# Performance work log

Measured on AMD Instinct MI355X. Metric: run time of the kernel, lower is better.

Reference implementation:

```python
import jax, jax.numpy as jnp
import numpy as np

# Synthetic layered DAG: 8 node-layers of width N -> 7 masked dense layers.
B = 4096        # batch
N = 2048        # nodes per DAG layer (= in_features = out_features)
DEPTH = 7       # number of weight layers (len(L) - 1)
DENSITY = 0.25  # fraction of predecessor edges present (mask sparsity)


def setup_inputs() -> dict:
    key = jax.random.key(0)
    kx, kw, km = jax.random.split(key, 3)
    x = jax.random.normal(kx, (B, N), dtype=jnp.float32)
    # Mask M: [DEPTH, N+1, N]; random 0/1 edges, last row (bias) all ones.
    m = (jax.random.uniform(km, (DEPTH, N + 1, N)) < DENSITY).astype(jnp.float32)
    M = m.at[:, -1, :].set(1.0)
    # Kaiming-uniform per column: bound = 1/sqrt(nnz_j) (torch code's init),
    # nonzero only at masked positions (W initialized to zeros elsewhere).
    nnz = jnp.maximum(M.sum(axis=1, keepdims=True), 1.0)  # [DEPTH,1,N]
    u = jax.random.uniform(kw, (DEPTH, N + 1, N), minval=-1.0, maxval=1.0)
    W = (u / jnp.sqrt(nnz)) * M
    return {"x": x, "W": W, "M": M}


def reference(x, W, M):
    # activations buffer semantics collapse to a per-layer chain because each
    # layer's preds are exactly the previous DAG layer; sinks = last layer.
    def step(acts, wm):
        w, m = wm  # [N+1, N] each
        h = jnp.concatenate(
            [acts, jnp.ones((acts.shape[0], 1), acts.dtype)], axis=1)  # [B, N+1]
        acts = jax.nn.relu(h @ (m * w))  # masked dense matmul + ReLU
        return acts, None

    out, _ = jax.lax.scan(step, x, (W, M))
    return out  # [B, N] activations of sink nodes
```

## Files before the change

### kernel.cpp

```cpp
#include <hip/hip_runtime.h>
#include <hip/hip_bf16.h>

typedef __bf16 bf16_t;
typedef __bf16 v8bf __attribute__((ext_vector_type(8)));
typedef __bf16 v4bf __attribute__((ext_vector_type(4)));
typedef float  v4f  __attribute__((ext_vector_type(4)));

#define B_ROWS 4096
#define N_COLS 2048
#define K_FULL 2049
#define K_PAD  2176
#define DEPTH  7

#define BM 128
#define BN 128
#define BK 64
#define NT (K_PAD / BK)

__global__ __launch_bounds__(256) void wt_kernel(const float* __restrict__ W,
                                                 bf16_t* __restrict__ Wt) {
  __shared__ float t[64][65];
  const int l  = blockIdx.z;
  const int k0 = blockIdx.x * 64;
  const int n0 = blockIdx.y * 64;
  const int tid = threadIdx.x;
  const int r  = tid >> 4;
  const int c4 = (tid & 15) * 4;
  const float* Wl = W + (size_t)l * K_FULL * N_COLS;
#pragma unroll
  for (int it = 0; it < 4; ++it) {
    const int k = k0 + r + it * 16;
    float4 v = make_float4(0.f, 0.f, 0.f, 0.f);
    if (k < K_FULL) v = *(const float4*)&Wl[(size_t)k * N_COLS + n0 + c4];
    t[c4 + 0][r + it * 16] = v.x;
    t[c4 + 1][r + it * 16] = v.y;
    t[c4 + 2][r + it * 16] = v.z;
    t[c4 + 3][r + it * 16] = v.w;
  }
  __syncthreads();
  bf16_t* Wtl = Wt + (size_t)l * N_COLS * K_PAD;
#pragma unroll
  for (int it = 0; it < 4; ++it) {
    const int n = r + it * 16;
    v4bf o;
    o[0] = (bf16_t)t[n][c4 + 0];
    o[1] = (bf16_t)t[n][c4 + 1];
    o[2] = (bf16_t)t[n][c4 + 2];
    o[3] = (bf16_t)t[n][c4 + 3];
    *(v4bf*)&Wtl[(size_t)(n0 + n) * K_PAD + k0 + c4] = o;
  }
}

__global__ __launch_bounds__(256) void init_kernel(const float* __restrict__ x,
                                                   bf16_t* __restrict__ A0,
                                                   bf16_t* __restrict__ A1) {
  const int c4 = (blockIdx.x * 256 + threadIdx.x) * 4;
  const int r  = blockIdx.y;
  if (c4 >= K_PAD) return;
  v4bf o;
  if (c4 < N_COLS) {
    const float4 v = *(const float4*)&x[(size_t)r * N_COLS + c4];
    o[0] = (bf16_t)v.x; o[1] = (bf16_t)v.y; o[2] = (bf16_t)v.z; o[3] = (bf16_t)v.w;
  } else {
    o[0] = (bf16_t)(c4 == N_COLS ? 1.0f : 0.0f);
    o[1] = (bf16_t)0.0f; o[2] = (bf16_t)0.0f; o[3] = (bf16_t)0.0f;
  }
  *(v4bf*)&A0[(size_t)r * K_PAD + c4] = o;
  if (c4 >= N_COLS) *(v4bf*)&A1[(size_t)r * K_PAD + c4] = o;
}

__global__ __launch_bounds__(256, 2) void gemm_kernel(
    const bf16_t* __restrict__ A, const bf16_t* __restrict__ Bt,
    bf16_t* __restrict__ Cn, float* __restrict__ Co) {
  __shared__ __align__(16) bf16_t As[2][BM * BK];
  __shared__ __align__(16) bf16_t Bs[2][BN * BK];

  const int tid  = threadIdx.x;
  const int wave = tid >> 6;
  const int lane = tid & 63;
  const int m0 = blockIdx.y * BM;
  const int n0 = blockIdx.x * BN;
  const int wm = (wave & 1) * 64;
  const int wn = (wave >> 1) * 64;
  const int quad = lane >> 4;
  const int l16  = lane & 15;

  int aoff[4], boff[4];
#pragma unroll
  for (int c = 0; c < 4; ++c) {
    const int gran = wave * 256 + c * 64 + lane;
    const int srow = gran >> 3;
    const int scol = ((gran & 7) ^ (srow & 7)) << 3;
    aoff[c] = (m0 + srow) * K_PAD + scol;
    boff[c] = (n0 + srow) * K_PAD + scol;
  }

  auto stage = [&](int buf, int kb) {
#pragma unroll
    for (int c = 0; c < 4; ++c) {
      __builtin_amdgcn_global_load_lds(
          (const __attribute__((address_space(1))) void*)(A + aoff[c] + kb),
          (__attribute__((address_space(3))) void*)((char*)&As[buf][0] + wave * 4096 + c * 1024),
          16, 0, 0);
    }
#pragma unroll
    for (int c = 0; c < 4; ++c) {
      __builtin_amdgcn_global_load_lds(
          (const __attribute__((address_space(1))) void*)(Bt + boff[c] + kb),
          (__attribute__((address_space(3))) void*)((char*)&Bs[buf][0] + wave * 4096 + c * 1024),
          16, 0, 0);
    }
  };

  v4f acc[4][4] = {};

  stage(0, 0);
  __syncthreads();

#pragma unroll 2
  for (int kt = 0; kt < NT; ++kt) {
    const int cur = kt & 1;
    if (kt + 1 < NT) stage(cur ^ 1, (kt + 1) * BK);

#pragma unroll
    for (int ks = 0; ks < 2; ++ks) {
      v8bf af[4], bfr[4];
      const int kg = ks * 4 + quad;
#pragma unroll
      for (int i = 0; i < 4; ++i) {
        const int arow = wm + i * 16 + l16;
        af[i] = *(const v8bf*)&As[cur][arow * BK + ((kg ^ (arow & 7)) << 3)];
      }
#pragma unroll
      for (int j = 0; j < 4; ++j) {
        const int brow = wn + j * 16 + l16;
        bfr[j] = *(const v8bf*)&Bs[cur][brow * BK + ((kg ^ (brow & 7)) << 3)];
      }
#pragma unroll
      for (int i = 0; i < 4; ++i)
#pragma unroll
        for (int j = 0; j < 4; ++j)
          acc[i][j] = __builtin_amdgcn_mfma_f32_16x16x32_bf16(af[i], bfr[j],
                                                              acc[i][j], 0, 0, 0);
    }
    __syncthreads();
  }

#pragma unroll
  for (int i = 0; i < 4; ++i) {
#pragma unroll
    for (int j = 0; j < 4; ++j) {
#pragma unroll
      for (int r = 0; r < 4; ++r) {
        float v = acc[i][j][r];
        v = v > 0.0f ? v : 0.0f;
        const int row = m0 + wm + i * 16 + quad * 4 + r;
        const int col = n0 + wn + j * 16 + l16;
        if (Co) Co[(size_t)row * N_COLS + col] = v;
        else    Cn[(size_t)row * K_PAD + col] = (bf16_t)v;
      }
    }
  }
}

extern "C" void kernel_launch(void* const* d_in, const int* in_sizes, int n_in,
                              void* d_out, int out_size, void* d_ws, size_t ws_size,
                              hipStream_t stream) {
  const float* x = (const float*)d_in[0];
  const float* W = (const float*)d_in[1];
  float* out = (float*)d_out;

  char* ws = (char*)d_ws;
  const size_t wtBytes = (size_t)DEPTH * N_COLS * K_PAD * sizeof(bf16_t);
  const size_t aBytes  = (size_t)B_ROWS * K_PAD * sizeof(bf16_t);
  bf16_t* Wt = (bf16_t*)ws;
  bf16_t* A0 = (bf16_t*)(ws + wtBytes);
  bf16_t* A1 = (bf16_t*)(ws + wtBytes + aBytes);

  wt_kernel<<<dim3(K_PAD / 64, N_COLS / 64, DEPTH), 256, 0, stream>>>(W, Wt);
  init_kernel<<<dim3((K_PAD / 4 + 255) / 256, B_ROWS), 256, 0, stream>>>(x, A0, A1);

  bf16_t* bufs[2] = {A0, A1};
  for (int l = 0; l < DEPTH; ++l) {
    const bf16_t* Ain = bufs[l & 1];
    bf16_t* Aout      = bufs[(l + 1) & 1];
    const bf16_t* Bl  = Wt + (size_t)l * N_COLS * K_PAD;
    const bool last   = (l == DEPTH - 1);
    gemm_kernel<<<dim3(N_COLS / BN, B_ROWS / BM), 256, 0, stream>>>(
        Ain, Bl, last ? nullptr : Aout, last ? out : nullptr);
  }
}
```

Measured before the change: 541.3 us.

## Use 128x256 tiles with 8 waves and half-K-tile software pipeline

The GEMM tile grows from 128x128 to 128x256, with 512 threads (8 waves) per block. Each K tile is staged in two 32-wide halves into a double buffer, so the next half-tile's global-to-LDS loads overlap the MFMAs, and explicit vmcnt waits and barriers replace the blanket syncthreads. A new quad-granular LDS swizzle and s_setprio around the MFMA block aim to cut bank conflicts and favour the math waves. The cost is 96KB of LDS per block, which may limit occupancy, plus fragile hand-written wait counts.

```diff
diff --git a/kernel.cpp b/kernel.cpp
--- a/kernel.cpp
+++ b/kernel.cpp
@@ -13,7 +13,7 @@
 #define DEPTH  7
 
 #define BM 128
-#define BN 128
+#define BN 256
 #define BK 64
 #define NT (K_PAD / BK)
 
@@ -69,82 +69,95 @@
   if (c4 >= N_COLS) *(v4bf*)&A1[(size_t)r * K_PAD + c4] = o;
 }
 
-__global__ __launch_bounds__(256, 2) void gemm_kernel(
+__global__ __launch_bounds__(512, 2) void gemm_kernel(
     const bf16_t* __restrict__ A, const bf16_t* __restrict__ Bt,
     bf16_t* __restrict__ Cn, float* __restrict__ Co) {
-  __shared__ __align__(16) bf16_t As[2][BM * BK];
-  __shared__ __align__(16) bf16_t Bs[2][BN * BK];
+  __shared__ __align__(16) char smem[2 * 49152];
 
   const int tid  = threadIdx.x;
   const int wave = tid >> 6;
   const int lane = tid & 63;
   const int m0 = blockIdx.y * BM;
   const int n0 = blockIdx.x * BN;
-  const int wm = (wave & 1) * 64;
-  const int wn = (wave >> 1) * 64;
+  const int wm = (wave >> 2) * 64;
+  const int wn = (wave & 3) * 64;
   const int quad = lane >> 4;
   const int l16  = lane & 15;
 
-  int aoff[4], boff[4];
-#pragma unroll
-  for (int c = 0; c < 4; ++c) {
-    const int gran = wave * 256 + c * 64 + lane;
-    const int srow = gran >> 3;
-    const int scol = ((gran & 7) ^ (srow & 7)) << 3;
-    aoff[c] = (m0 + srow) * K_PAD + scol;
-    boff[c] = (n0 + srow) * K_PAD + scol;
-  }
-
-  auto stage = [&](int buf, int kb) {
-#pragma unroll
-    for (int c = 0; c < 4; ++c) {
-      __builtin_amdgcn_global_load_lds(
-          (const __attribute__((address_space(1))) void*)(A + aoff[c] + kb),
-          (__attribute__((address_space(3))) void*)((char*)&As[buf][0] + wave * 4096 + c * 1024),
-          16, 0, 0);
-    }
-#pragma unroll
-    for (int c = 0; c < 4; ++c) {
-      __builtin_amdgcn_global_load_lds(
-          (const __attribute__((address_space(1))) void*)(Bt + boff[c] + kb),
-          (__attribute__((address_space(3))) void*)((char*)&Bs[buf][0] + wave * 4096 + c * 1024),
-          16, 0, 0);
-    }
+  auto qg = [](int r, int kq) {
+    return (r >> 1) * 8 + (r & 1) * 4 + (kq ^ ((r >> 1) & 3));
   };
+  int a_off[4], b_off[4];
+#pragma unroll
+  for (int i = 0; i < 4; ++i) a_off[i] = qg(wm + i * 16 + l16, quad) * 16;
+#pragma unroll
+  for (int j = 0; j < 4; ++j) b_off[j] = qg(wn + j * 16 + l16, quad) * 16;
+
+  const int r_s  = 2 * (tid >> 3) + ((tid >> 2) & 1);
+  const int kq_s = (tid & 3) ^ ((tid >> 3) & 3);
+  const size_t aoff  = (size_t)(m0 + r_s) * K_PAD + kq_s * 8;
+  const size_t boff0 = (size_t)(n0 + r_s) * K_PAD + kq_s * 8;
+  const size_t boff1 = boff0 + (size_t)128 * K_PAD;
+
+  auto stageHalf = [&](int dbuf, int dhalf, int tile) {
+    const int sA = dbuf * 49152 + dhalf * 8192 + wave * 1024;
+    const int sB = dbuf * 49152 + 16384 + dhalf * 16384 + wave * 1024;
+    const size_t e = (size_t)tile * 64 + dhalf * 32;
+    __builtin_amdgcn_global_load_lds(
+        (const __attribute__((address_space(1))) void*)(A + aoff + e),
+        (__attribute__((address_space(3))) void*)(smem + sA), 16, 0, 0);
+    __builtin_amdgcn_global_load_lds(
+        (const __attribute__((address_space(1))) void*)(Bt + boff0 + e),
+        (__attribute__((address_space(3))) void*)(smem + sB), 16, 0, 0);
+    __builtin_amdgcn_global_load_lds(
+        (const __attribute__((address_space(1))) void*)(Bt + boff1 + e),
+        (__attribute__((address_space(3))) void*)(smem + sB + 8192), 16, 0, 0);
+  };
 
   v4f acc[4][4] = {};
 
-  stage(0, 0);
-  __syncthreads();
-
-#pragma unroll 2
-  for (int kt = 0; kt < NT; ++kt) {
-    const int cur = kt & 1;
-    if (kt + 1 < NT) stage(cur ^ 1, (kt + 1) * BK);
-
-#pragma unroll
-    for (int ks = 0; ks < 2; ++ks) {
-      v8bf af[4], bfr[4];
-      const int kg = ks * 4 + quad;
-#pragma unroll
-      for (int i = 0; i < 4; ++i) {
-        const int arow = wm + i * 16 + l16;
-        af[i] = *(const v8bf*)&As[cur][arow * BK + ((kg ^ (arow & 7)) << 3)];
-      }
-#pragma unroll
-      for (int j = 0; j < 4; ++j) {
-        const int brow = wn + j * 16 + l16;
-        bfr[j] = *(const v8bf*)&Bs[cur][brow * BK + ((kg ^ (brow & 7)) << 3)];
-      }
-#pragma unroll
-      for (int i = 0; i < 4; ++i)
-#pragma unroll
-        for (int j = 0; j < 4; ++j)
-          acc[i][j] = __builtin_amdgcn_mfma_f32_16x16x32_bf16(af[i], bfr[j],
-                                                              acc[i][j], 0, 0, 0);
-    }
-    __syncthreads();
-  }
+  auto phase = [&](int buf, int khalf, bool doStage, int sBuf, int sHalf,
+                   int sTile, int vm) {
+    const char* ab = smem + buf * 49152 + khalf * 8192;
+    const char* bb = smem + buf * 49152 + 16384 + khalf * 16384;
+    v8bf af[4], bf[4];
+#pragma unroll
+    for (int i = 0; i < 4; ++i) af[i] = *(const v8bf*)(ab + a_off[i]);
+#pragma unroll
+    for (int j = 0; j < 4; ++j) bf[j] = *(const v8bf*)(bb + b_off[j]);
+    if (doStage) stageHalf(sBuf, sHalf, sTile);
+    asm volatile("s_barrier" ::: "memory");
+    __builtin_amdgcn_s_setprio(1);
+#pragma unroll
+    for (int i = 0; i < 4; ++i)
+#pragma unroll
+      for (int j = 0; j < 4; ++j)
+        acc[i][j] = __builtin_amdgcn_mfma_f32_16x16x32_bf16(af[i], bf[j],
+                                                            acc[i][j], 0, 0, 0);
+    __builtin_amdgcn_s_setprio(0);
+    asm volatile("s_waitcnt lgkmcnt(0)" ::: "memory");
+    if (vm == 6)      asm volatile("s_waitcnt vmcnt(6)" ::: "memory");
+    else if (vm == 3) asm volatile("s_waitcnt vmcnt(3)" ::: "memory");
+    else if (vm == 0) asm volatile("s_waitcnt vmcnt(0)" ::: "memory");
+    if (vm >= 0) asm volatile("s_barrier" ::: "memory");
+  };
+
+  stageHalf(0, 0, 0);
+  stageHalf(0, 1, 0);
+  stageHalf(1, 0, 1);
+  asm volatile("s_waitcnt vmcnt(6)" ::: "memory");
+  asm volatile("s_barrier" ::: "memory");
+
+#pragma unroll 1
+  for (int kt = 0; kt < NT - 2; ++kt) {
+    const int b = kt & 1;
+    phase(b, 0, true, b ^ 1, 1, kt + 1, 6);
+    phase(b, 1, true, b, 0, kt + 2, 6);
+  }
+  phase(0, 0, true, 1, 1, NT - 1, 6);
+  phase(0, 1, false, 0, 0, 0, 3);
+  phase(1, 0, false, 0, 0, 0, 0);
+  phase(1, 1, false, 0, 0, 0, -1);
 
 #pragma unroll
   for (int i = 0; i < 4; ++i) {
@@ -186,7 +199,7 @@
     bf16_t* Aout      = bufs[(l + 1) & 1];
     const bf16_t* Bl  = Wt + (size_t)l * N_COLS * K_PAD;
     const bool last   = (l == DEPTH - 1);
-    gemm_kernel<<<dim3(N_COLS / BN, B_ROWS / BM), 256, 0, stream>>>(
+    gemm_kernel<<<dim3(N_COLS / BN, B_ROWS / BM), 512, 0, stream>>>(
         Ain, Bl, last ? nullptr : Aout, last ? out : nullptr);
   }
 }
```

After: 536.7 us. Within noise of the previous version (-0.8%).
